# Kernel optimization log

Measured on AMD Instinct MI355X. Metric: run time of the kernel, lower is better.

## Reference

```python
import jax, jax.numpy as jnp
import numpy as np

# BinarizeConv2dSDP hyperparameters (from init_kwargs): SDP rank K and output scale.
SCALE = 1.0
K = 2
EPS = 1e-5  # BatchNorm2d default eps


@jax.custom_vjp
def binarize(x):
    # deterministic sign binarization (1-bit)
    return jnp.sign(x)

def _bin_fwd(x):
    return jnp.sign(x), x

def _bin_bwd(x, g):
    # straight-through estimator with hardtanh clipping, as in standard BNN training
    return (g * (jnp.abs(x) <= 1.0).astype(g.dtype),)

binarize.defvjp(_bin_fwd, _bin_bwd)


def conv3x3(x, w, stride=1):
    # x: [N, C, H, W], w: [O, I, 3, 3], padding=1
    return jax.lax.conv_general_dilated(
        x, w,
        window_strides=(stride, stride),
        padding=((1, 1), (1, 1)),
        dimension_numbers=("NCHW", "OIHW", "NCHW"),
    )


def binconv(x, w, stride=1):
    # binarized-input, binarized-weight conv with SDP scale
    return conv3x3(binarize(x), binarize(w), stride) * (SCALE / K)


def batchnorm(x, gamma, beta):
    # training-mode BatchNorm2d over (N, H, W)
    m = jnp.mean(x, axis=(0, 2, 3), keepdims=True)
    v = jnp.var(x, axis=(0, 2, 3), keepdims=True)
    xn = (x - m) * jax.lax.rsqrt(v + EPS)
    return xn * gamma[None, :, None, None] + beta[None, :, None, None]


def setup_inputs() -> dict:
    key = jax.random.key(0)
    k1, k2, k3 = jax.random.split(key, 3)
    N, C, H, W = 32, 256, 56, 56
    x = jax.random.normal(k1, (N, C, H, W), dtype=jnp.float32)
    w1 = jax.random.normal(k2, (C, C, 3, 3), dtype=jnp.float32) * 0.05
    w2 = jax.random.normal(k3, (C, C, 3, 3), dtype=jnp.float32) * 0.05
    g1 = jnp.ones((C,), jnp.float32)
    b1 = jnp.zeros((C,), jnp.float32)
    g2 = jnp.ones((C,), jnp.float32)
    b2 = jnp.zeros((C,), jnp.float32)
    return {"x": x, "w1": w1, "g1": g1, "b1": b1, "w2": w2, "g2": g2, "b2": b2}


def reference(x, w1, g1, b1, w2, g2, b2):
    # out = hardtanh(bn1(conv1(x)))
    out = jnp.clip(batchnorm(binconv(x, w1, 1), g1, b1), -1.0, 1.0)
    # out = bn2(conv2(out)) + shortcut(x)  (identity shortcut: stride=1, in_planes==planes)
    out = batchnorm(binconv(out, w2, 1), g2, b2) + x
    # final hardtanh
    return jnp.clip(out, -1.0, 1.0)
```

## Files before the change

### kernel.cpp

```cpp
#include <hip/hip_runtime.h>
#include <stdint.h>

#define NB    32
#define C     256
#define HH    56
#define WW    56
#define HW    3136
#define P_TOT 100352
#define PW    58
#define PHW   3364
#define NPAD  107648
#define EPSBN 1e-5f

__device__ __forceinline__ uint64_t shflx64(uint64_t v, int m) {
    int lo = __shfl_xor((int)(uint32_t)v, m, 64);
    int hi = __shfl_xor((int)(uint32_t)(v >> 32), m, 64);
    return ((uint64_t)(uint32_t)hi << 32) | (uint32_t)lo;
}
__device__ __forceinline__ uint64_t bt64(uint64_t M, int lane) {
    const uint64_t mk[6] = {0x5555555555555555ULL, 0x3333333333333333ULL,
                            0x0F0F0F0F0F0F0F0FULL, 0x00FF00FF00FF00FFULL,
                            0x0000FFFF0000FFFFULL, 0x00000000FFFFFFFFULL};
#pragma unroll
    for (int k = 0; k < 6; ++k) {
        int s = 1 << k;
        uint64_t mA = mk[k];
        uint64_t v = shflx64(M, s);
        M = (lane & s) ? ((M & ~mA) | ((v & ~mA) >> s))
                       : ((M &  mA) | ((v &  mA) << s));
    }
    return M;
}

__global__ __launch_bounds__(256) void zero_misc(uint64_t* __restrict__ px1,
                                                 uint64_t* __restrict__ px2,
                                                 int* __restrict__ sS1,
                                                 unsigned long long* __restrict__ sQ1,
                                                 int* __restrict__ sS2,
                                                 unsigned long long* __restrict__ sQ2) {
    int idx = blockIdx.x * 256 + threadIdx.x;
    if (idx < 256) { sS1[idx] = 0; sQ1[idx] = 0; sS2[idx] = 0; sQ2[idx] = 0; }
    if (idx >= NPAD) return;
    int pp = idx % PHW;
    int ph = pp / PW, pw_ = pp - ph * PW;
    if (ph == 0 || ph == PW - 1 || pw_ == 0 || pw_ == PW - 1) {
#pragma unroll
        for (int wd = 0; wd < 4; ++wd) {
            px1[(size_t)wd * NPAD + idx] = 0ull;
            px2[(size_t)wd * NPAD + idx] = 0ull;
        }
    }
}

__global__ __launch_bounds__(256) void pack_wgt(const float* __restrict__ w1,
                                                const float* __restrict__ w2,
                                                uint64_t* __restrict__ pw1,
                                                uint64_t* __restrict__ pw2,
                                                int* __restrict__ pc1,
                                                int* __restrict__ pc2) {
    int gw = blockIdx.x * 4 + (threadIdx.x >> 6);
    int lane = threadIdx.x & 63;
    int set = gw / 9216;
    int r = gw - set * 9216;
    int wd = r & 3, q = r >> 2;
    int t = q % 9, co = q / 9;
    const float* w = set ? w2 : w1;
    float v = w[(size_t)co * 2304 + (size_t)(wd * 64 + lane) * 9 + t];
    unsigned long long m = __ballot(v >= 0.0f);
    if (lane == 0) {
        uint64_t* pw = set ? pw2 : pw1;
        int* pc = set ? pc2 : pc1;
        pw[(size_t)(wd * 9 + t) * 256 + co] = m;
        pc[(co * 9 + t) * 4 + wd] = (int)__popcll(m);
    }
}

__global__ __launch_bounds__(256) void build_K(const int* __restrict__ pc1,
                                               const int* __restrict__ pc2,
                                               unsigned short* __restrict__ K1,
                                               unsigned short* __restrict__ K2) {
    int tid = blockIdx.x * 256 + threadIdx.x;
    int set = tid / 2304;
    int r = tid - set * 2304;
    int pat = r >> 8, co = r & 255;
    int pv = pat / 3, pq = pat - pv * 3;
    const int* pc = set ? pc2 : pc1;
    int k = 0, corr = 0;
#pragma unroll
    for (int t = 0; t < 9; ++t) {
        int ty = t / 3, tx = t - ty * 3;
        bool inv = (pv == 0 && ty == 0) || (pv == 2 && ty == 2) ||
                   (pq == 0 && tx == 0) || (pq == 2 && tx == 2);
        if (inv) {
            ++k;
            const int* p = pc + (co * 9 + t) * 4;
            corr += p[0] + p[1] + p[2] + p[3];
        }
    }
    unsigned short* K = set ? K2 : K1;
    K[pat * 256 + co] = (unsigned short)(256 * (9 - k) + 2 * corr);
}

__global__ __launch_bounds__(256) void pack_act(const float* __restrict__ x,
                                                uint64_t* __restrict__ px) {
    int wid = blockIdx.x * 4 + (threadIdx.x >> 6);
    int lane = threadIdx.x & 63;
    int wd = wid & 3;
    int g = wid >> 2;
    int n = g / 49, gi = g - n * 49;
    const float* xp = x + ((size_t)n * C + wd * 64) * HW + gi * 64 + lane;
    uint64_t M = 0;
#pragma unroll
    for (int c = 0; c < 64; ++c) {
        float v = xp[(size_t)c * HW];
        unsigned long long m = __ballot(v >= 0.0f);
        if (lane == c) M = m;
    }
    M = bt64(M, lane);
    int p = gi * 64 + lane;
    int h = p / WW, w = p - h * WW;
    px[(size_t)wd * NPAD + (size_t)n * PHW + (size_t)(h + 1) * PW + (w + 1)] = M;
}

__global__ __launch_bounds__(256, 4) void bconv(const uint64_t* __restrict__ px,
                                                const uint64_t* __restrict__ pw,
                                                const unsigned short* __restrict__ Kt,
                                                short* __restrict__ sout,
                                                int* __restrict__ sS,
                                                unsigned long long* __restrict__ sQ) {
    __shared__ unsigned short Kl[2304];
    int co = threadIdx.x;
#pragma unroll 1
    for (int i = threadIdx.x; i < 2304; i += 256) Kl[i] = Kt[i];

    uint64_t wv[4][9];
#pragma unroll
    for (int wd = 0; wd < 4; ++wd)
#pragma unroll
        for (int t = 0; t < 9; ++t)
            wv[wd][t] = pw[(size_t)(wd * 9 + t) * 256 + co];
    __syncthreads();

    int row = blockIdx.x;
    int n = row / HH, h = row - n * HH;
    size_t base = (size_t)n * PHW + (size_t)(h + 1) * PW + 1;
    short* orow = sout + (size_t)(n * HW + h * WW) * C + co;
    const bool irow = (h > 0) && (h < HH - 1);
    int pv = (h == 0) ? 0 : ((h == HH - 1) ? 2 : 1);

    int ssum = 0, ssq = 0;
#pragma unroll 2
    for (int w = 0; w < WW; ++w) {
        int acc = 0;
#pragma unroll
        for (int wd = 0; wd < 4; ++wd) {
            const uint64_t* xb = px + (size_t)wd * NPAD + base + w;
            uint64_t t0 = xb[-PW - 1], t1 = xb[-PW], t2 = xb[-PW + 1];
            uint64_t t3 = xb[-1],      t4 = xb[0],   t5 = xb[1];
            uint64_t t6 = xb[PW - 1],  t7 = xb[PW],  t8 = xb[PW + 1];
            int r = 0;
            r += __popcll(t0 ^ wv[wd][0]);
            r += __popcll(t1 ^ wv[wd][1]);
            r += __popcll(t2 ^ wv[wd][2]);
            r += __popcll(t3 ^ wv[wd][3]);
            r += __popcll(t4 ^ wv[wd][4]);
            r += __popcll(t5 ^ wv[wd][5]);
            r += __popcll(t6 ^ wv[wd][6]);
            r += __popcll(t7 ^ wv[wd][7]);
            r += __popcll(t8 ^ wv[wd][8]);
            acc += r;
        }
        int dot;
        if (irow && w > 0 && w < WW - 1) {
            dot = 2304 - 2 * acc;
        } else {
            int pq = (w == 0) ? 0 : ((w == WW - 1) ? 2 : 1);
            dot = (int)Kl[(pv * 3 + pq) * 256 + co] - 2 * acc;
        }
        orow[(size_t)w * C] = (short)dot;
        ssum += dot;
        ssq += dot * dot;
    }
    atomicAdd(sS + co, ssum);
    atomicAdd(sQ + co, (unsigned long long)(unsigned int)ssq);
}

__global__ __launch_bounds__(256) void bnAB(const int* __restrict__ sS,
                                            const unsigned long long* __restrict__ sQ,
                                            const float* __restrict__ g,
                                            const float* __restrict__ b,
                                            float* __restrict__ A,
                                            float* __restrict__ Bv) {
    int c = threadIdx.x;
    float S = (float)sS[c];
    float Q = (float)sQ[c];
    float m  = 0.5f  * S / (float)P_TOT;
    float e2 = 0.25f * Q / (float)P_TOT;
    float var = e2 - m * m;
    float a = g[c] * rsqrtf(var + EPSBN);
    A[c]  = 0.5f * a;
    Bv[c] = b[c] - m * a;
}

__global__ __launch_bounds__(256) void bnpack(const short* __restrict__ s,
                                              const float* __restrict__ A,
                                              const float* __restrict__ Bv,
                                              uint64_t* __restrict__ px) {
    int p = blockIdx.x * 256 + threadIdx.x;
    const int4* sp = (const int4*)(s + (size_t)p * C);
    uint32_t bits[8];
#pragma unroll
    for (int wd = 0; wd < 8; ++wd) bits[wd] = 0u;
#pragma unroll 4
    for (int j = 0; j < 32; ++j) {
        int4 v = sp[j];
#pragma unroll
        for (int k = 0; k < 4; ++k) {
            int u = (&v.x)[k];
            int c = j * 8 + k * 2;
            float y0 = (float)(short)(u & 0xFFFF) * A[c] + Bv[c];
            float y1 = (float)(u >> 16) * A[c + 1] + Bv[c + 1];
            if (y0 >= 0.0f) bits[c >> 5] |= (1u << (c & 31));
            if (y1 >= 0.0f) bits[(c + 1) >> 5] |= (1u << ((c + 1) & 31));
        }
    }
    int n = p / HW, rem = p - n * HW;
    int h = rem / WW, w = rem - h * WW;
    size_t pidx = (size_t)n * PHW + (size_t)(h + 1) * PW + (w + 1);
#pragma unroll
    for (int wd = 0; wd < 4; ++wd)
        px[(size_t)wd * NPAD + pidx] =
            ((uint64_t)bits[2 * wd + 1] << 32) | bits[2 * wd];
}

__global__ __launch_bounds__(256) void finalize(const short* __restrict__ s,
                                                const float* __restrict__ x,
                                                const float* __restrict__ A,
                                                const float* __restrict__ Bv,
                                                float* __restrict__ out) {
    __shared__ int4 lds4[2048];
    int tid = threadIdx.x;
    int p0 = blockIdx.x * 64;
    int n = p0 / HW, rem0 = p0 - n * HW;
    const int4* s4 = (const int4*)(s + (size_t)p0 * C);
#pragma unroll
    for (int it = 0; it < 8; ++it) {
        int u = tid + it * 256;
        int r = u >> 5, j = u & 31;
        int4 v = s4[r * 32 + j];
        lds4[r * 32 + ((j + r) & 31)] = v;
    }
    __syncthreads();
    int lane = tid & 63;
    int wvn = tid >> 6;
#pragma unroll 4
    for (int it = 0; it < 64; ++it) {
        int c = it * 4 + wvn;
        int slot = ((c >> 3) + lane) & 31;
        short sv = ((const short*)lds4)[lane * 256 + slot * 8 + (c & 7)];
        size_t gi = ((size_t)n * C + c) * HW + rem0 + lane;
        float y = (float)sv * A[c] + Bv[c] + x[gi];
        out[gi] = fminf(1.0f, fmaxf(-1.0f, y));
    }
}

extern "C" void kernel_launch(void* const* d_in, const int* in_sizes, int n_in,
                              void* d_out, int out_size, void* d_ws, size_t ws_size,
                              hipStream_t stream) {
    const float* x  = (const float*)d_in[0];
    const float* w1 = (const float*)d_in[1];
    const float* g1 = (const float*)d_in[2];
    const float* b1 = (const float*)d_in[3];
    const float* w2 = (const float*)d_in[4];
    const float* g2 = (const float*)d_in[5];
    const float* b2 = (const float*)d_in[6];
    float* out = (float*)d_out;

    char* ws = (char*)d_ws;
    uint64_t* pw1 = (uint64_t*)ws;            ws += 4 * 9 * 256 * 8;
    uint64_t* pw2 = (uint64_t*)ws;            ws += 4 * 9 * 256 * 8;
    int* pc1 = (int*)ws;                      ws += 9216 * 4;
    int* pc2 = (int*)ws;                      ws += 9216 * 4;
    unsigned short* K1 = (unsigned short*)ws; ws += 8192;
    unsigned short* K2 = (unsigned short*)ws; ws += 8192;
    float* A1 = (float*)ws;                   ws += 1024;
    float* B1 = (float*)ws;                   ws += 1024;
    float* A2 = (float*)ws;                   ws += 1024;
    float* B2 = (float*)ws;                   ws += 1024;
    int* sS1 = (int*)ws;                      ws += 1024;
    int* sS2 = (int*)ws;                      ws += 1024;
    unsigned long long* sQ1 = (unsigned long long*)ws; ws += 2048;
    unsigned long long* sQ2 = (unsigned long long*)ws; ws += 2048;
    uint64_t* px1 = (uint64_t*)ws;            ws += (size_t)4 * NPAD * 8;
    uint64_t* px2 = (uint64_t*)ws;            ws += (size_t)4 * NPAD * 8;
    short* s16 = (short*)ws;

    zero_misc<<<(NPAD + 255) / 256, 256, 0, stream>>>(px1, px2, sS1, sQ1, sS2, sQ2);
    pack_wgt<<<4608, 256, 0, stream>>>(w1, w2, pw1, pw2, pc1, pc2);
    build_K<<<18, 256, 0, stream>>>(pc1, pc2, K1, K2);
    pack_act<<<1568, 256, 0, stream>>>(x, px1);

    bconv<<<NB * HH, 256, 0, stream>>>(px1, pw1, K1, s16, sS1, sQ1);
    bnAB<<<1, 256, 0, stream>>>(sS1, sQ1, g1, b1, A1, B1);
    bnpack<<<P_TOT / 256, 256, 0, stream>>>(s16, A1, B1, px2);

    bconv<<<NB * HH, 256, 0, stream>>>(px2, pw2, K2, s16, sS2, sQ2);
    bnAB<<<1, 256, 0, stream>>>(sS2, sQ2, g2, b2, A2, B2);

    finalize<<<P_TOT / 64, 256, 0, stream>>>(s16, x, A2, B2, out);
}
```

Baseline: 539.4 us.

## Interleave packed activations, slide bconv window in registers, fuse BN stats into consumers

Packed activations move from a word-major layout to a per-pixel interleaved layout holding four 64-bit words, and weights move to a per-output-channel layout. bconv now keeps a sliding 3x3 window in registers, so each step loads only the new column instead of all nine taps, and its occupancy hint drops to 2 blocks. The bnAB kernel is removed: BN scale and shift are recomputed inside bnpack and finalize. zero_misc is folded into build_K and pack_act, and bnpack now builds its bits with ballot and transpose. The changes aim to cut kernel launches and redundant loads, at the cost of more register pressure in bconv.

```diff
diff --git a/kernel.cpp b/kernel.cpp
--- a/kernel.cpp
+++ b/kernel.cpp
@@ -30,26 +30,6 @@
                        : ((M &  mA) | ((v &  mA) << s));
     }
     return M;
-}
-
-__global__ __launch_bounds__(256) void zero_misc(uint64_t* __restrict__ px1,
-                                                 uint64_t* __restrict__ px2,
-                                                 int* __restrict__ sS1,
-                                                 unsigned long long* __restrict__ sQ1,
-                                                 int* __restrict__ sS2,
-                                                 unsigned long long* __restrict__ sQ2) {
-    int idx = blockIdx.x * 256 + threadIdx.x;
-    if (idx < 256) { sS1[idx] = 0; sQ1[idx] = 0; sS2[idx] = 0; sQ2[idx] = 0; }
-    if (idx >= NPAD) return;
-    int pp = idx % PHW;
-    int ph = pp / PW, pw_ = pp - ph * PW;
-    if (ph == 0 || ph == PW - 1 || pw_ == 0 || pw_ == PW - 1) {
-#pragma unroll
-        for (int wd = 0; wd < 4; ++wd) {
-            px1[(size_t)wd * NPAD + idx] = 0ull;
-            px2[(size_t)wd * NPAD + idx] = 0ull;
-        }
-    }
 }
 
 __global__ __launch_bounds__(256) void pack_wgt(const float* __restrict__ w1,
@@ -70,7 +50,7 @@
     if (lane == 0) {
         uint64_t* pw = set ? pw2 : pw1;
         int* pc = set ? pc2 : pc1;
-        pw[(size_t)(wd * 9 + t) * 256 + co] = m;
+        pw[(size_t)co * 40 + wd * 9 + t] = m;
         pc[(co * 9 + t) * 4 + wd] = (int)__popcll(m);
     }
 }
@@ -78,8 +58,18 @@
 __global__ __launch_bounds__(256) void build_K(const int* __restrict__ pc1,
                                                const int* __restrict__ pc2,
                                                unsigned short* __restrict__ K1,
-                                               unsigned short* __restrict__ K2) {
+                                               unsigned short* __restrict__ K2,
+                                               int* __restrict__ sS1,
+                                               unsigned long long* __restrict__ sQ1,
+                                               int* __restrict__ sS2,
+                                               unsigned long long* __restrict__ sQ2) {
+    if (blockIdx.x == 18) {
+        int t = threadIdx.x;
+        sS1[t] = 0; sQ1[t] = 0; sS2[t] = 0; sQ2[t] = 0;
+        return;
+    }
     int tid = blockIdx.x * 256 + threadIdx.x;
+    if (tid >= 4608) return;
     int set = tid / 2304;
     int r = tid - set * 2304;
     int pat = r >> 8, co = r & 255;
@@ -102,144 +92,165 @@
 }
 
 __global__ __launch_bounds__(256) void pack_act(const float* __restrict__ x,
-                                                uint64_t* __restrict__ px) {
-    int wid = blockIdx.x * 4 + (threadIdx.x >> 6);
+                                                uint64_t* __restrict__ px1,
+                                                uint64_t* __restrict__ px2) {
+    if (blockIdx.x >= 392) {
+        int u = (blockIdx.x - 392) * 256 + threadIdx.x;
+        if (u >= 29184) return;
+        int wd = u & 3, v = u >> 2;
+        int n = v / 228, cell = v - n * 228;
+        int ph, pw_;
+        if (cell < 58)       { ph = 0;          pw_ = cell; }
+        else if (cell < 116) { ph = 57;         pw_ = cell - 58; }
+        else if (cell < 172) { ph = cell - 115; pw_ = 0; }
+        else                 { ph = cell - 171; pw_ = 57; }
+        size_t idx = ((size_t)n * PHW + (size_t)ph * PW + pw_) * 4 + wd;
+        px1[idx] = 0ull;
+        px2[idx] = 0ull;
+        return;
+    }
+    int g = blockIdx.x * 4 + (threadIdx.x >> 6);
     int lane = threadIdx.x & 63;
-    int wd = wid & 3;
-    int g = wid >> 2;
     int n = g / 49, gi = g - n * 49;
-    const float* xp = x + ((size_t)n * C + wd * 64) * HW + gi * 64 + lane;
-    uint64_t M = 0;
-#pragma unroll
-    for (int c = 0; c < 64; ++c) {
-        float v = xp[(size_t)c * HW];
-        unsigned long long m = __ballot(v >= 0.0f);
-        if (lane == c) M = m;
-    }
-    M = bt64(M, lane);
+    const float* xp = x + (size_t)n * C * HW + gi * 64 + lane;
+    uint64_t M[4];
+#pragma unroll
+    for (int wd = 0; wd < 4; ++wd) {
+        uint64_t Mq = 0;
+#pragma unroll
+        for (int c = 0; c < 64; ++c) {
+            float v = xp[(size_t)(wd * 64 + c) * HW];
+            unsigned long long m = __ballot(v >= 0.0f);
+            if (lane == c) Mq = m;
+        }
+        M[wd] = bt64(Mq, lane);
+    }
     int p = gi * 64 + lane;
     int h = p / WW, w = p - h * WW;
-    px[(size_t)wd * NPAD + (size_t)n * PHW + (size_t)(h + 1) * PW + (w + 1)] = M;
-}
-
-__global__ __launch_bounds__(256, 4) void bconv(const uint64_t* __restrict__ px,
-                                                const uint64_t* __restrict__ pw,
+    uint64_t* dst = px1 + ((size_t)n * PHW + (size_t)(h + 1) * PW + (w + 1)) * 4;
+    ((ulonglong2*)dst)[0] = make_ulonglong2(M[0], M[1]);
+    ((ulonglong2*)dst)[1] = make_ulonglong2(M[2], M[3]);
+}
+
+__global__ __launch_bounds__(256, 2) void bconv(const uint64_t* __restrict__ px,
+                                                const uint64_t* __restrict__ pwt,
                                                 const unsigned short* __restrict__ Kt,
                                                 short* __restrict__ sout,
                                                 int* __restrict__ sS,
                                                 unsigned long long* __restrict__ sQ) {
-    __shared__ unsigned short Kl[2304];
     int co = threadIdx.x;
-#pragma unroll 1
-    for (int i = threadIdx.x; i < 2304; i += 256) Kl[i] = Kt[i];
-
-    uint64_t wv[4][9];
-#pragma unroll
-    for (int wd = 0; wd < 4; ++wd)
-#pragma unroll
-        for (int t = 0; t < 9; ++t)
-            wv[wd][t] = pw[(size_t)(wd * 9 + t) * 256 + co];
-    __syncthreads();
+    uint64_t wv[36];
+    const volatile uint64_t* wq = (const volatile uint64_t*)(pwt + (size_t)co * 40);
+#pragma unroll
+    for (int i = 0; i < 36; ++i) wv[i] = wq[i];
 
     int row = blockIdx.x;
     int n = row / HH, h = row - n * HH;
-    size_t base = (size_t)n * PHW + (size_t)(h + 1) * PW + 1;
+    int pv = (h == 0) ? 0 : ((h == HH - 1) ? 2 : 1);
+    int K0 = Kt[(pv * 3 + 0) * 256 + co];
+    int K1 = Kt[(pv * 3 + 1) * 256 + co];
+    int K2 = Kt[(pv * 3 + 2) * 256 + co];
+
+    const uint64_t* base = px + (size_t)(n * PHW + h * PW) * 4;
     short* orow = sout + (size_t)(n * HW + h * WW) * C + co;
-    const bool irow = (h > 0) && (h < HH - 1);
-    int pv = (h == 0) ? 0 : ((h == HH - 1) ? 2 : 1);
+
+    uint64_t cA[12], cB[12], cC[12];
+#pragma unroll
+    for (int k = 0; k < 3; ++k)
+#pragma unroll
+        for (int wd = 0; wd < 4; ++wd) {
+            cA[k * 4 + wd] = base[(size_t)(k * PW + 0) * 4 + wd];
+            cB[k * 4 + wd] = base[(size_t)(k * PW + 1) * 4 + wd];
+        }
 
     int ssum = 0, ssq = 0;
-#pragma unroll 2
+#pragma unroll 4
     for (int w = 0; w < WW; ++w) {
+#pragma unroll
+        for (int k = 0; k < 3; ++k)
+#pragma unroll
+            for (int wd = 0; wd < 4; ++wd)
+                cC[k * 4 + wd] = base[(size_t)(k * PW + w + 2) * 4 + wd];
         int acc = 0;
 #pragma unroll
-        for (int wd = 0; wd < 4; ++wd) {
-            const uint64_t* xb = px + (size_t)wd * NPAD + base + w;
-            uint64_t t0 = xb[-PW - 1], t1 = xb[-PW], t2 = xb[-PW + 1];
-            uint64_t t3 = xb[-1],      t4 = xb[0],   t5 = xb[1];
-            uint64_t t6 = xb[PW - 1],  t7 = xb[PW],  t8 = xb[PW + 1];
-            int r = 0;
-            r += __popcll(t0 ^ wv[wd][0]);
-            r += __popcll(t1 ^ wv[wd][1]);
-            r += __popcll(t2 ^ wv[wd][2]);
-            r += __popcll(t3 ^ wv[wd][3]);
-            r += __popcll(t4 ^ wv[wd][4]);
-            r += __popcll(t5 ^ wv[wd][5]);
-            r += __popcll(t6 ^ wv[wd][6]);
-            r += __popcll(t7 ^ wv[wd][7]);
-            r += __popcll(t8 ^ wv[wd][8]);
-            acc += r;
-        }
-        int dot;
-        if (irow && w > 0 && w < WW - 1) {
-            dot = 2304 - 2 * acc;
-        } else {
-            int pq = (w == 0) ? 0 : ((w == WW - 1) ? 2 : 1);
-            dot = (int)Kl[(pv * 3 + pq) * 256 + co] - 2 * acc;
-        }
+        for (int k = 0; k < 3; ++k)
+#pragma unroll
+            for (int wd = 0; wd < 4; ++wd) {
+                acc += __popcll(cA[k * 4 + wd] ^ wv[wd * 9 + k * 3 + 0]);
+                acc += __popcll(cB[k * 4 + wd] ^ wv[wd * 9 + k * 3 + 1]);
+                acc += __popcll(cC[k * 4 + wd] ^ wv[wd * 9 + k * 3 + 2]);
+            }
+        int Ksel = (w == 0) ? K0 : ((w == WW - 1) ? K2 : K1);
+        int dot = Ksel - 2 * acc;
         orow[(size_t)w * C] = (short)dot;
         ssum += dot;
-        ssq += dot * dot;
+        ssq  += dot * dot;
+#pragma unroll
+        for (int i = 0; i < 12; ++i) { cA[i] = cB[i]; cB[i] = cC[i]; }
     }
     atomicAdd(sS + co, ssum);
     atomicAdd(sQ + co, (unsigned long long)(unsigned int)ssq);
 }
 
-__global__ __launch_bounds__(256) void bnAB(const int* __restrict__ sS,
-                                            const unsigned long long* __restrict__ sQ,
-                                            const float* __restrict__ g,
-                                            const float* __restrict__ b,
-                                            float* __restrict__ A,
-                                            float* __restrict__ Bv) {
-    int c = threadIdx.x;
-    float S = (float)sS[c];
-    float Q = (float)sQ[c];
-    float m  = 0.5f  * S / (float)P_TOT;
-    float e2 = 0.25f * Q / (float)P_TOT;
-    float var = e2 - m * m;
-    float a = g[c] * rsqrtf(var + EPSBN);
-    A[c]  = 0.5f * a;
-    Bv[c] = b[c] - m * a;
-}
-
 __global__ __launch_bounds__(256) void bnpack(const short* __restrict__ s,
-                                              const float* __restrict__ A,
-                                              const float* __restrict__ Bv,
+                                              const int* __restrict__ sS,
+                                              const unsigned long long* __restrict__ sQ,
+                                              const float* __restrict__ g,
+                                              const float* __restrict__ b,
                                               uint64_t* __restrict__ px) {
-    int p = blockIdx.x * 256 + threadIdx.x;
-    const int4* sp = (const int4*)(s + (size_t)p * C);
-    uint32_t bits[8];
-#pragma unroll
-    for (int wd = 0; wd < 8; ++wd) bits[wd] = 0u;
-#pragma unroll 4
-    for (int j = 0; j < 32; ++j) {
-        int4 v = sp[j];
-#pragma unroll
-        for (int k = 0; k < 4; ++k) {
-            int u = (&v.x)[k];
-            int c = j * 8 + k * 2;
-            float y0 = (float)(short)(u & 0xFFFF) * A[c] + Bv[c];
-            float y1 = (float)(u >> 16) * A[c + 1] + Bv[c + 1];
-            if (y0 >= 0.0f) bits[c >> 5] |= (1u << (c & 31));
-            if (y1 >= 0.0f) bits[(c + 1) >> 5] |= (1u << ((c + 1) & 31));
+    int gq = blockIdx.x * 4 + (threadIdx.x >> 6);
+    int lane = threadIdx.x & 63;
+    float Aq[4], Bq[4];
+#pragma unroll
+    for (int wd = 0; wd < 4; ++wd) {
+        int c = wd * 64 + lane;
+        float S = (float)sS[c];
+        float Q = (float)sQ[c];
+        float m  = 0.5f  * S / (float)P_TOT;
+        float e2 = 0.25f * Q / (float)P_TOT;
+        float a = g[c] * rsqrtf(e2 - m * m + EPSBN);
+        Aq[wd] = 0.5f * a;
+        Bq[wd] = b[c] - m * a;
+    }
+    int n = gq / 49, gi = gq - n * 49;
+    int P0 = n * HW + gi * 64;
+    uint64_t M[4] = {0, 0, 0, 0};
+#pragma unroll 2
+    for (int pi = 0; pi < 64; ++pi) {
+        const short* sp = s + (size_t)(P0 + pi) * C + lane;
+#pragma unroll
+        for (int wd = 0; wd < 4; ++wd) {
+            float y = (float)sp[wd * 64] * Aq[wd] + Bq[wd];
+            unsigned long long m = __ballot(y >= 0.0f);
+            if (lane == pi) M[wd] = m;
         }
     }
-    int n = p / HW, rem = p - n * HW;
-    int h = rem / WW, w = rem - h * WW;
-    size_t pidx = (size_t)n * PHW + (size_t)(h + 1) * PW + (w + 1);
-#pragma unroll
-    for (int wd = 0; wd < 4; ++wd)
-        px[(size_t)wd * NPAD + pidx] =
-            ((uint64_t)bits[2 * wd + 1] << 32) | bits[2 * wd];
+    int p = gi * 64 + lane;
+    int h = p / WW, w = p - h * WW;
+    uint64_t* dst = px + ((size_t)n * PHW + (size_t)(h + 1) * PW + (w + 1)) * 4;
+    ((ulonglong2*)dst)[0] = make_ulonglong2(M[0], M[1]);
+    ((ulonglong2*)dst)[1] = make_ulonglong2(M[2], M[3]);
 }
 
 __global__ __launch_bounds__(256) void finalize(const short* __restrict__ s,
                                                 const float* __restrict__ x,
-                                                const float* __restrict__ A,
-                                                const float* __restrict__ Bv,
+                                                const int* __restrict__ sS,
+                                                const unsigned long long* __restrict__ sQ,
+                                                const float* __restrict__ g,
+                                                const float* __restrict__ b,
                                                 float* __restrict__ out) {
+    __shared__ float sA[256], sB[256];
     __shared__ int4 lds4[2048];
     int tid = threadIdx.x;
+    {
+        float S = (float)sS[tid];
+        float Q = (float)sQ[tid];
+        float m  = 0.5f  * S / (float)P_TOT;
+        float e2 = 0.25f * Q / (float)P_TOT;
+        float a = g[tid] * rsqrtf(e2 - m * m + EPSBN);
+        sA[tid] = 0.5f * a;
+        sB[tid] = b[tid] - m * a;
+    }
     int p0 = blockIdx.x * 64;
     int n = p0 / HW, rem0 = p0 - n * HW;
     const int4* s4 = (const int4*)(s + (size_t)p0 * C);
@@ -247,20 +258,18 @@
     for (int it = 0; it < 8; ++it) {
         int u = tid + it * 256;
         int r = u >> 5, j = u & 31;
-        int4 v = s4[r * 32 + j];
-        lds4[r * 32 + ((j + r) & 31)] = v;
+        lds4[r * 32 + ((j + r) & 31)] = s4[r * 32 + j];
     }
     __syncthreads();
-    int lane = tid & 63;
-    int wvn = tid >> 6;
+    int lane = tid & 63, wvn = tid >> 6;
 #pragma unroll 4
     for (int it = 0; it < 64; ++it) {
         int c = it * 4 + wvn;
         int slot = ((c >> 3) + lane) & 31;
         short sv = ((const short*)lds4)[lane * 256 + slot * 8 + (c & 7)];
         size_t gi = ((size_t)n * C + c) * HW + rem0 + lane;
-        float y = (float)sv * A[c] + Bv[c] + x[gi];
-        out[gi] = fminf(1.0f, fmaxf(-1.0f, y));
+        float yv = (float)sv * sA[c] + sB[c] + x[gi];
+        out[gi] = fminf(1.0f, fmaxf(-1.0f, yv));
     }
 }
 
@@ -277,16 +286,12 @@
     float* out = (float*)d_out;
 
     char* ws = (char*)d_ws;
-    uint64_t* pw1 = (uint64_t*)ws;            ws += 4 * 9 * 256 * 8;
-    uint64_t* pw2 = (uint64_t*)ws;            ws += 4 * 9 * 256 * 8;
+    uint64_t* pwt1 = (uint64_t*)ws;           ws += 256 * 40 * 8;
+    uint64_t* pwt2 = (uint64_t*)ws;           ws += 256 * 40 * 8;
     int* pc1 = (int*)ws;                      ws += 9216 * 4;
     int* pc2 = (int*)ws;                      ws += 9216 * 4;
     unsigned short* K1 = (unsigned short*)ws; ws += 8192;
     unsigned short* K2 = (unsigned short*)ws; ws += 8192;
-    float* A1 = (float*)ws;                   ws += 1024;
-    float* B1 = (float*)ws;                   ws += 1024;
-    float* A2 = (float*)ws;                   ws += 1024;
-    float* B2 = (float*)ws;                   ws += 1024;
     int* sS1 = (int*)ws;                      ws += 1024;
     int* sS2 = (int*)ws;                      ws += 1024;
     unsigned long long* sQ1 = (unsigned long long*)ws; ws += 2048;
@@ -295,17 +300,14 @@
     uint64_t* px2 = (uint64_t*)ws;            ws += (size_t)4 * NPAD * 8;
     short* s16 = (short*)ws;
 
-    zero_misc<<<(NPAD + 255) / 256, 256, 0, stream>>>(px1, px2, sS1, sQ1, sS2, sQ2);
-    pack_wgt<<<4608, 256, 0, stream>>>(w1, w2, pw1, pw2, pc1, pc2);
-    build_K<<<18, 256, 0, stream>>>(pc1, pc2, K1, K2);
-    pack_act<<<1568, 256, 0, stream>>>(x, px1);
-
-    bconv<<<NB * HH, 256, 0, stream>>>(px1, pw1, K1, s16, sS1, sQ1);
-    bnAB<<<1, 256, 0, stream>>>(sS1, sQ1, g1, b1, A1, B1);
-    bnpack<<<P_TOT / 256, 256, 0, stream>>>(s16, A1, B1, px2);
-
-    bconv<<<NB * HH, 256, 0, stream>>>(px2, pw2, K2, s16, sS2, sQ2);
-    bnAB<<<1, 256, 0, stream>>>(sS2, sQ2, g2, b2, A2, B2);
-
-    finalize<<<P_TOT / 64, 256, 0, stream>>>(s16, x, A2, B2, out);
-}
+    pack_wgt<<<4608, 256, 0, stream>>>(w1, w2, pwt1, pwt2, pc1, pc2);
+    build_K<<<19, 256, 0, stream>>>(pc1, pc2, K1, K2, sS1, sQ1, sS2, sQ2);
+    pack_act<<<392 + 114, 256, 0, stream>>>(x, px1, px2);
+
+    bconv<<<NB * HH, 256, 0, stream>>>(px1, pwt1, K1, s16, sS1, sQ1);
+    bnpack<<<392, 256, 0, stream>>>(s16, sS1, sQ1, g1, b1, px2);
+
+    bconv<<<NB * HH, 256, 0, stream>>>(px2, pwt2, K2, s16, sS2, sQ2);
+
+    finalize<<<1568, 256, 0, stream>>>(s16, x, sS2, sQ2, g2, b2, out);
+}
```

Result: slower. 601.0 us (+11.4%).
